# Kernel optimization log

Measured on AMD Instinct MI355X. Metric: run time of the kernel, lower is better.

## Reference

```python
import jax, jax.numpy as jnp
import numpy as np

S, B, N, L, ND = 16, 64, 10000, 128, 1  # seq_len, batch, nodes, latent_dim, node_dim


def setup_inputs() -> dict:
    key = jax.random.key(0)
    ks = jax.random.split(key, 20)
    D_msg = ND + L        # GRU input: [node_feat || time_enc]
    D_h = ND + 2 * L      # attention input: [x || memory || time_enc]
    g = lambda k, shp, s: (jax.random.normal(k, shp, jnp.float32) * s)
    return {
        "x": jax.random.normal(ks[0], (S, B, N, ND), jnp.float32),
        "t": jax.random.uniform(ks[1], (S, B, N, 1), jnp.float32),
        "source": jax.random.randint(ks[2], (S, B, 1), 0, N),
        "target": jax.random.randint(ks[3], (S, B, 1), 0, N),
        "neighbor_mask": jax.random.randint(ks[4], (S, B, N), 0, 2).astype(jnp.bool_),
        # TimeEncoder: cos(t @ w + b)
        "time_w": g(ks[5], (1, L), 1.0),
        "time_b": g(ks[6], (L,), 1.0),
        # MemoryUpdater: GRUCell(input=D_msg, hidden=L)
        "W_ih": g(ks[7], (3 * L, D_msg), 1.0 / np.sqrt(D_msg)),
        "W_hh": g(ks[8], (3 * L, L), 1.0 / np.sqrt(L)),
        "b_ih": jnp.zeros((3 * L,), jnp.float32),
        "b_hh": jnp.zeros((3 * L,), jnp.float32),
        # Attention projections (D_h -> L)
        "Wq": g(ks[9], (D_h, L), 1.0 / np.sqrt(D_h)),
        "bq": jnp.zeros((L,), jnp.float32),
        "Wk": g(ks[10], (D_h, L), 1.0 / np.sqrt(D_h)),
        "bk": jnp.zeros((L,), jnp.float32),
        "Wv": g(ks[11], (D_h, L), 1.0 / np.sqrt(D_h)),
        "bv": jnp.zeros((L,), jnp.float32),
        # final Linear(L -> 1)
        "W_out": g(ks[12], (L, 1), 1.0 / np.sqrt(L)),
        "b_out": jnp.zeros((1,), jnp.float32),
    }


def reference(x, t, source, target, neighbor_mask, time_w, time_b,
              W_ih, W_hh, b_ih, b_hh, Wq, bq, Wk, bk, Wv, bv, W_out, b_out):
    s_len, bsz, n_nodes, _ = x.shape
    lat = time_w.shape[1]
    scale = 1.0 / jnp.sqrt(jnp.float32(lat))
    bidx = jnp.arange(bsz)

    def time_enc(tt):  # [..., 1] -> [..., L]
        return jnp.cos(tt @ time_w + time_b)

    def gru(msg, h):  # torch GRUCell semantics
        gi = msg @ W_ih.T + b_ih
        gh = h @ W_hh.T + b_hh
        i_r, i_z, i_n = jnp.split(gi, 3, axis=-1)
        h_r, h_z, h_n = jnp.split(gh, 3, axis=-1)
        r = jax.nn.sigmoid(i_r + h_r)
        z = jax.nn.sigmoid(i_z + h_z)
        n = jnp.tanh(i_n + r * h_n)
        return (1.0 - z) * n + z * h

    def step(memory, batch):
        xb, tb, src, tgt, mask = batch
        src = src[:, 0]
        tgt = tgt[:, 0]
        dt = time_enc(tb)  # [B, N, L]
        # 1. update memory at source and target nodes
        msg_s = jnp.concatenate([xb[bidx, src], dt[bidx, src]], axis=-1)  # [B, ND+L]
        msg_t = jnp.concatenate([xb[bidx, tgt], dt[bidx, tgt]], axis=-1)
        new_s = gru(msg_s, memory[src])
        new_t = gru(msg_t, memory[tgt])
        mem = memory.at[src].set(new_s).at[tgt].set(new_t)
        # 2. embedding: target query
        tvec = jnp.concatenate([xb[bidx, tgt], mem[tgt]], axis=-1)  # [B, ND+L]
        enc0 = jnp.broadcast_to(jnp.cos(time_b), (bsz, lat))  # time_enc(t=0)
        target_h = jnp.concatenate([tvec, enc0], axis=-1)  # [B, ND+2L]
        # per-node keys/values
        h = jnp.concatenate(
            [xb, jnp.broadcast_to(mem, (bsz, n_nodes, lat)), dt], axis=-1)  # [B, N, ND+2L]
        q = target_h @ Wq + bq          # [B, L]
        k = h @ Wk + bk                 # [B, N, L]
        v = h @ Wv + bv                 # [B, N, L]
        scores = jnp.einsum("bl,bnl->bn", q, k) * scale
        scores = jnp.where(mask, scores, jnp.float32(-1e9))
        attn = jax.nn.softmax(scores, axis=-1)
        z = jnp.einsum("bn,bnl->bl", attn, v)
        logit = z @ W_out + b_out       # [B, 1]
        return mem, logit

    mem0 = jnp.zeros((n_nodes, lat), jnp.float32)
    _, logits = jax.lax.scan(step, mem0, (x, t, source, target, neighbor_mask))
    return logits  # [S, B, 1]
```

## Files before the change

### kernel.cpp

```cpp
#include <hip/hip_runtime.h>
#include <math.h>

#define S_LEN 16
#define BSZ   64
#define NN    10000
#define LAT   128
#define DH    257
#define KTAB  1024
#define CSTRIDE (KTAB + 8)
#define FSTRIDE (KTAB + 4)
#define NTILE 64
#define NTILES 157
#define SCALE 0.08838834764831845f
#define NEG1E9 -1000000000.0f

__global__ __launch_bounds__(256) void setup_all_kernel(
    const float* __restrict__ W_ih, const float* __restrict__ W_hh,
    const float* __restrict__ tw, const float* __restrict__ tb_,
    const float* __restrict__ Wq, const float* __restrict__ bq,
    const float* __restrict__ Wv, const float* __restrict__ bv,
    const float* __restrict__ W_out, const float* __restrict__ b_out,
    const int* __restrict__ mask,
    float* __restrict__ W_ihT, float* __restrict__ W_hhT,
    float* __restrict__ costab, float* __restrict__ wv_out, float* __restrict__ vconst,
    float* __restrict__ qconst, int* __restrict__ modep) {
    int blk = blockIdx.x, tid = threadIdx.x;
    if (blk < 256) {
        int gtid = blk * 256 + tid;
        const int GS = 256 * 256;
        for (int i = gtid; i < 129 * 384; i += GS) { int d = i / 384, j = i % 384; W_ihT[i] = W_ih[j * 129 + d]; }
        for (int i = gtid; i < 128 * 384; i += GS) { int l = i / 384, j = i % 384; W_hhT[i] = W_hh[j * 128 + l]; }
        for (int p = gtid; p <= KTAB; p += GS) {
            float tv = (float)p * (1.0f / KTAB);
            for (int l = 0; l < 128; ++l) costab[l * CSTRIDE + p] = __cosf(tv * tw[l] + tb_[l]);
        }
    } else {
        for (int d = tid; d < DH; d += 256) {
            float a = 0.f;
            for (int j = 0; j < LAT; ++j) a += Wv[d * LAT + j] * W_out[j];
            wv_out[d] = a;
        }
        if (tid == 0) {
            float a = b_out[0];
            for (int j = 0; j < LAT; ++j) a += bv[j] * W_out[j];
            *vconst = a;
        }
        if (tid < 128) {
            float a = bq[tid];
            for (int j = 0; j < 128; ++j) a += __cosf(tb_[j]) * Wq[(129 + j) * LAT + tid];
            qconst[tid] = a;
        }
        __shared__ int hasHigh, hasFloat;
        if (tid == 0) { hasHigh = 0; hasFloat = 0; }
        __syncthreads();
        for (int i = tid; i < 4096; i += 256) {
            int v = mask[i];
            if ((unsigned)v > 1u) atomicOr(&hasHigh, 1);
            if (v == 0x3F800000) atomicOr(&hasFloat, 1);
        }
        __syncthreads();
        if (tid == 0) *modep = hasFloat ? 2 : (hasHigh ? 1 : 0);
    }
}

__global__ __launch_bounds__(256) void setup2_kernel(
    const float* __restrict__ Wk, const float* __restrict__ Wq,
    const float* __restrict__ bk, const float* __restrict__ qconst,
    float* __restrict__ BT, float* __restrict__ uc, float* __restrict__ kw0,
    float* __restrict__ abk, float* __restrict__ scal) {
    int blk = blockIdx.x, tid = threadIdx.x;
    __shared__ float vrow[128];
    if (blk < 128) {
        int l = blk;
        if (tid < 128) vrow[tid] = Wq[(1 + l) * LAT + tid];
        __syncthreads();
        for (int d = tid; d < DH; d += 256) {
            const float* wkr = Wk + d * LAT;
            float a = 0.f;
#pragma unroll 4
            for (int j = 0; j < 128; ++j) a += wkr[j] * vrow[j];
            BT[l * 260 + d] = a;
        }
    } else if (blk == 128) {
        if (tid < 128) vrow[tid] = qconst[tid];
        __syncthreads();
        for (int d = tid; d < DH; d += 256) {
            const float* wkr = Wk + d * LAT;
            float a = 0.f;
#pragma unroll 4
            for (int j = 0; j < 128; ++j) a += wkr[j] * vrow[j];
            uc[d] = a;
        }
    } else if (blk == 129) {
        if (tid < 128) vrow[tid] = Wq[tid];
        __syncthreads();
        for (int d = tid; d < DH; d += 256) {
            const float* wkr = Wk + d * LAT;
            float a = 0.f;
#pragma unroll 4
            for (int j = 0; j < 128; ++j) a += wkr[j] * vrow[j];
            kw0[d] = a;
        }
    } else {
        if (tid < 128) vrow[tid] = bk[tid];
        __syncthreads();
        if (tid < 128) {
            const float* wqr = Wq + (1 + tid) * LAT;
            float a = 0.f;
#pragma unroll 4
            for (int j = 0; j < 128; ++j) a += wqr[j] * vrow[j];
            abk[tid] = a;
        } else if (tid == 128) {
            float a = 0.f;
            for (int j = 0; j < 128; ++j) a += qconst[j] * bk[j];
            scal[0] = a;
        } else if (tid == 129) {
            float a = 0.f;
            for (int j = 0; j < 128; ++j) a += Wq[j] * bk[j];
            scal[1] = a;
        }
    }
}

__device__ __forceinline__ void do_gru_row256(int r, int tid2, int s,
    const float* __restrict__ x, const float* __restrict__ t,
    const int* __restrict__ source, const int* __restrict__ target,
    const float* __restrict__ tw, const float* __restrict__ tb_,
    const float* __restrict__ W_ihT, const float* __restrict__ W_hhT,
    const float* __restrict__ b_ih, const float* __restrict__ b_hh,
    const float* __restrict__ mem, float* __restrict__ newh, float* sm) {
    float* msg = sm;
    float* h   = sm + 132;
    float* gi3 = sm + 260;
    float* gh3 = sm + 644;
    int b = r & 63;
    int idx = (r < 64) ? source[s * BSZ + b] : target[s * BSZ + b];
    const float* xs = x + (size_t)(s * BSZ + b) * NN;
    const float* ts = t + (size_t)(s * BSZ + b) * NN;
    if (tid2 == 0) msg[0] = xs[idx];
    if (tid2 < 128) {
        float tv = ts[idx];
        msg[1 + tid2] = __cosf(tv * tw[tid2] + tb_[tid2]);
        h[tid2] = mem[(size_t)idx * LAT + tid2];
    }
    __syncthreads();
    if (tid2 < 128) {
        int j = tid2;
        float a0 = b_ih[j], a1 = b_ih[128 + j], a2 = b_ih[256 + j];
#pragma unroll 4
        for (int d = 0; d < 129; ++d) {
            float m = msg[d];
            const float* col = W_ihT + d * 384;
            a0 += m * col[j]; a1 += m * col[128 + j]; a2 += m * col[256 + j];
        }
        gi3[j] = a0; gi3[128 + j] = a1; gi3[256 + j] = a2;
    } else {
        int j = tid2 - 128;
        float a0 = b_hh[j], a1 = b_hh[128 + j], a2 = b_hh[256 + j];
#pragma unroll 4
        for (int l = 0; l < 128; ++l) {
            float hv = h[l];
            const float* col = W_hhT + l * 384;
            a0 += hv * col[j]; a1 += hv * col[128 + j]; a2 += hv * col[256 + j];
        }
        gh3[j] = a0; gh3[128 + j] = a1; gh3[256 + j] = a2;
    }
    __syncthreads();
    if (tid2 < 128) {
        int j = tid2;
        float rr = 1.f / (1.f + __expf(-(gi3[j] + gh3[j])));
        float zz = 1.f / (1.f + __expf(-(gi3[128 + j] + gh3[128 + j])));
        float nn2 = tanhf(gi3[256 + j] + rr * gh3[256 + j]);
        newh[r * LAT + j] = (1.f - zz) * nn2 + zz * h[j];
    }
}

__global__ __launch_bounds__(256) void pre_kernel(
    const float* __restrict__ x, const float* __restrict__ t,
    const int* __restrict__ source, const int* __restrict__ target,
    const float* __restrict__ tw, const float* __restrict__ tb_,
    const float* __restrict__ W_ihT, const float* __restrict__ W_hhT,
    const float* __restrict__ b_ih, const float* __restrict__ b_hh,
    const float* __restrict__ mem, float* __restrict__ newh,
    const float* __restrict__ wv_out, const float* __restrict__ costab,
    float* __restrict__ gtab) {
    __shared__ __align__(16) float sm[1028];
    int blk = blockIdx.x, tid = threadIdx.x;
    if (blk < 5) {
        __shared__ float wv_s[LAT];
        if (tid < LAT) wv_s[tid] = wv_out[129 + tid];
        __syncthreads();
        int p = blk * 256 + tid;
        if (p <= KTAB) {
            float a = 0.f;
            for (int l = 0; l < 128; ++l) a += wv_s[l] * costab[l * CSTRIDE + p];
            gtab[p] = a;
        }
        return;
    }
    int r = blk - 5;
    do_gru_row256(r, tid, 0, x, t, source, target, tw, tb_,
                  W_ihT, W_hhT, b_ih, b_hh, mem, newh, sm);
}

__device__ __forceinline__ void do_combine(const float* __restrict__ partials,
                                           const float* __restrict__ vconst,
                                           float* __restrict__ out, int ps, int tid) {
    if (tid >= 64) return;
    int b = tid;
    float M = -3.0e38f, D = 0.f, Nm = 0.f;
    const float4* pp = (const float4*)partials + b * NTILES;
    for (int i = 0; i < NTILES; ++i) {
        float4 p = pp[i];
        float M2 = fmaxf(M, p.x);
        float e1 = __expf(M - M2), e2 = __expf(p.x - M2);
        D = D * e1 + p.y * e2;
        Nm = Nm * e1 + p.z * e2;
        M = M2;
    }
    out[ps * BSZ + b] = Nm / D + vconst[0];
}

__global__ __launch_bounds__(512) void step_a3_kernel(
    const float* __restrict__ x, const int* __restrict__ source, const int* __restrict__ target,
    const float* __restrict__ BT, const float* __restrict__ uc, const float* __restrict__ kw0,
    const float* __restrict__ abk, const float* __restrict__ scal,
    const float* __restrict__ newh, float* __restrict__ mem,
    float* __restrict__ u0_g, float* __restrict__ qbk_g, float* __restrict__ uT,
    float* __restrict__ ftab, const float* __restrict__ costab,
    const float* __restrict__ partials, const float* __restrict__ vconst,
    float* __restrict__ out, int s) {
    int blk = blockIdx.x;
    int tid = threadIdx.x;
    if (blk == 64) {
        __shared__ int idxs[128];
        __shared__ int alive[128];
        if (tid < 128) idxs[tid] = (tid < 64) ? source[s * BSZ + tid] : target[s * BSZ + (tid - 64)];
        __syncthreads();
        if (tid < 128) {
            int i2 = idxs[tid];
            int a = 1;
            for (int r2 = tid + 1; r2 < 128; ++r2)
                if (idxs[r2] == i2) { a = 0; break; }
            alive[tid] = a;
        }
        __syncthreads();
        int row = tid >> 2, q4 = tid & 3;
        if (alive[row]) {
            const float4* srcp = (const float4*)(newh + row * LAT + q4 * 32);
            float4* dstp = (float4*)(mem + (size_t)idxs[row] * LAT + q4 * 32);
#pragma unroll
            for (int j = 0; j < 8; ++j) dstp[j] = srcp[j];
        }
        return;
    }
    if (blk == 65) {
        if (s > 0) do_combine(partials, vconst, out, s - 1, tid);
        return;
    }
    int b = blk;
    __shared__ float memv[128];
    __shared__ float udt_s[128];
    __shared__ float upart[4][260];
    __shared__ float red[8];
    __shared__ __align__(16) float fpart[3 * 1024];
    __shared__ int s_last;
    __shared__ float xvs;
    if (tid < 64) {
        unsigned long long mball = __ballot(target[s * BSZ + tid] == target[s * BSZ + b]);
        if (tid == 0) {
            s_last = 63 - __builtin_clzll(mball);
            xvs = x[(size_t)(s * BSZ + b) * NN + target[s * BSZ + b]];
        }
    }
    __syncthreads();
    if (tid < 128) memv[tid] = newh[(64 + s_last) * LAT + tid];
    __syncthreads();
    float xv = xvs;
    {
        int dd = tid & 127, kc = tid >> 7;
        int l0 = kc * 32;
        for (int d = dd; d < DH; d += 128) {
            float a = 0.f;
#pragma unroll 4
            for (int l = l0; l < l0 + 32; ++l) a += memv[l] * BT[l * 260 + d];
            upart[kc][d] = a;
        }
    }
    __syncthreads();
    if (tid < 257) {
        float a = uc[tid] + xv * kw0[tid] + upart[0][tid] + upart[1][tid] + upart[2][tid] + upart[3][tid];
        if (tid == 0) u0_g[b] = a;
        else if (tid <= 128) uT[(tid - 1) * BSZ + b] = a;
        else udt_s[tid - 129] = a;
    }
    if (tid >= 448) {
        int i = tid - 448;
        float a = memv[i] * abk[i] + memv[64 + i] * abk[64 + i];
        for (int off = 32; off; off >>= 1) a += __shfl_down(a, off, 64);
        if (i == 0) qbk_g[b] = scal[0] + xv * scal[1] + a;
    }
    __syncthreads();
    {
        int pi = tid & 127, lc = tid >> 7;
        int l0 = lc * 32;
        float a0x = 0.f, a0y = 0.f, a0z = 0.f, a0w = 0.f;
        float a1x = 0.f, a1y = 0.f, a1z = 0.f, a1w = 0.f;
#pragma unroll 4
        for (int l = l0; l < l0 + 32; ++l) {
            float ul = udt_s[l];
            const float* cp = &costab[l * CSTRIDE + pi * 8];
            float4 c0 = *(const float4*)cp;
            float4 c1 = *(const float4*)(cp + 4);
            a0x += ul * c0.x; a0y += ul * c0.y; a0z += ul * c0.z; a0w += ul * c0.w;
            a1x += ul * c1.x; a1y += ul * c1.y; a1z += ul * c1.z; a1w += ul * c1.w;
        }
        if (lc) {
            float* fp = &fpart[(lc - 1) * 1024 + pi * 8];
            *(float4*)fp = make_float4(a0x, a0y, a0z, a0w);
            *(float4*)(fp + 4) = make_float4(a1x, a1y, a1z, a1w);
        }
        if (pi == 127) {
            float a = 0.f;
            for (int l = l0; l < l0 + 32; ++l) a += udt_s[l] * costab[l * CSTRIDE + KTAB];
            red[lc] = a;
        }
        __syncthreads();
        if (lc == 0) {
            for (int c = 0; c < 3; ++c) {
                const float* fp = &fpart[c * 1024 + pi * 8];
                a0x += fp[0]; a0y += fp[1]; a0z += fp[2]; a0w += fp[3];
                a1x += fp[4]; a1y += fp[5]; a1z += fp[6]; a1w += fp[7];
            }
            float* fo = &ftab[b * FSTRIDE + pi * 8];
            *(float4*)fo = make_float4(a0x, a0y, a0z, a0w);
            *(float4*)(fo + 4) = make_float4(a1x, a1y, a1z, a1w);
        }
        if (tid == 0) ftab[b * FSTRIDE + KTAB] = red[0] + red[1] + red[2] + red[3];
    }
}

__global__ __launch_bounds__(256) void step_b2_kernel(
    const float* __restrict__ x, const float* __restrict__ t,
    const void* __restrict__ maskp, const int* __restrict__ modep,
    const int* __restrict__ source, const int* __restrict__ target,
    const float* __restrict__ tw, const float* __restrict__ tb_,
    const float* __restrict__ W_ihT, const float* __restrict__ W_hhT,
    const float* __restrict__ b_ih, const float* __restrict__ b_hh,
    const float* __restrict__ mem, float* __restrict__ newh,
    const float* __restrict__ uT, const float* __restrict__ u0_g,
    const float* __restrict__ qbk_g, const float* __restrict__ ftab,
    const float* __restrict__ gtab, const float* __restrict__ wv_out,
    float* __restrict__ partials, int s) {
    int blk = blockIdx.x, tid = threadIdx.x;

    __shared__ float memT[64 * 72];
    __shared__ float uTs[64 * 68];
    __shared__ float memv_s[64];
    __shared__ float wv_s[128];
    __shared__ float u0_s[64], qbk_s[64];

    if (blk >= NTILES) {
        if (s < S_LEN - 1) {
            int r = blk - NTILES;
            do_gru_row256(r, tid, s + 1, x, t, source, target, tw, tb_,
                          W_ihT, W_hhT, b_ih, b_hh, mem, newh, memT );
        }
        return;
    }

    int tile = blk;
    int n0 = tile * NTILE;
    int tb = tid >> 4, tn = tid & 15;
    int nvalid = NN - n0; if (nvalid > NTILE) nvalid = NTILE;

    if (tid < 128) wv_s[tid] = wv_out[1 + tid];
    if (tid < 64) { u0_s[tid] = u0_g[tid]; qbk_s[tid] = qbk_g[tid]; memv_s[tid] = 0.f; }

    float acc[4][4];
#pragma unroll
    for (int i = 0; i < 4; ++i)
#pragma unroll
        for (int j = 0; j < 4; ++j) acc[i][j] = 0.f;

    for (int l0 = 0; l0 < 128; l0 += 64) {
        __syncthreads();
        {
            int n_l = tid & 63, lq = (tid >> 6) * 16;
            if (n_l < nvalid) {
                const float* mrow = mem + (size_t)(n0 + n_l) * LAT + l0 + lq;
                float4 a0 = *(const float4*)(mrow + 0);
                float4 a1 = *(const float4*)(mrow + 4);
                float4 a2 = *(const float4*)(mrow + 8);
                float4 a3 = *(const float4*)(mrow + 12);
                memT[(lq + 0) * 72 + n_l] = a0.x; memT[(lq + 1) * 72 + n_l] = a0.y;
                memT[(lq + 2) * 72 + n_l] = a0.z; memT[(lq + 3) * 72 + n_l] = a0.w;
                memT[(lq + 4) * 72 + n_l] = a1.x; memT[(lq + 5) * 72 + n_l] = a1.y;
                memT[(lq + 6) * 72 + n_l] = a1.z; memT[(lq + 7) * 72 + n_l] = a1.w;
                memT[(lq + 8) * 72 + n_l] = a2.x; memT[(lq + 9) * 72 + n_l] = a2.y;
                memT[(lq + 10) * 72 + n_l] = a2.z; memT[(lq + 11) * 72 + n_l] = a2.w;
                memT[(lq + 12) * 72 + n_l] = a3.x; memT[(lq + 13) * 72 + n_l] = a3.y;
                memT[(lq + 14) * 72 + n_l] = a3.z; memT[(lq + 15) * 72 + n_l] = a3.w;
            } else {
                for (int j = 0; j < 16; ++j) memT[(lq + j) * 72 + n_l] = 0.f;
            }
        }
        {
            int bq4 = (tid & 15) * 4;
            int ll = (tid >> 4) * 4;
            for (int j = 0; j < 4; ++j) {
                float4 v = *(const float4*)&uT[(l0 + ll + j) * BSZ + bq4];
                *(float4*)&uTs[(ll + j) * 68 + bq4] = v;
            }
        }
        __syncthreads();
        if (tid < 64) {
            float a = memv_s[tid];
            for (int l = 0; l < 64; ++l) a += wv_s[l0 + l] * memT[l * 72 + tid];
            memv_s[tid] = a;
        }
        for (int l = 0; l < 64; ++l) {
            float4 uv = *(const float4*)&uTs[l * 68 + tb * 4];
            float4 mv = *(const float4*)&memT[l * 72 + tn * 4];
            acc[0][0] += uv.x * mv.x; acc[0][1] += uv.x * mv.y; acc[0][2] += uv.x * mv.z; acc[0][3] += uv.x * mv.w;
            acc[1][0] += uv.y * mv.x; acc[1][1] += uv.y * mv.y; acc[1][2] += uv.y * mv.z; acc[1][3] += uv.y * mv.w;
            acc[2][0] += uv.z * mv.x; acc[2][1] += uv.z * mv.y; acc[2][2] += uv.z * mv.z; acc[2][3] += uv.z * mv.w;
            acc[3][0] += uv.w * mv.x; acc[3][1] += uv.w * mv.y; acc[3][2] += uv.w * mv.z; acc[3][3] += uv.w * mv.w;
        }
    }
    __syncthreads();

    const float c0 = wv_out[0];
    int mode = *modep;
    const int* m32 = (const int*)maskp;
    const unsigned char* m8 = (const unsigned char*)maskp;
    const float* mf = (const float*)maskp;

    float pm[4], pd[4], pn[4];
#pragma unroll
    for (int i = 0; i < 4; ++i) { pm[i] = -3.0e38f; pd[i] = 0.f; pn[i] = 0.f; }

    for (int i = 0; i < 4; ++i) {
        int b = tb * 4 + i;
        size_t base = (size_t)(s * BSZ + b) * NN + n0 + tn * 4;
        float xv4[4], tv4[4]; int msk[4], vld[4];
        if (tn * 4 + 3 < nvalid) {
            float4 xx = *(const float4*)(x + base);
            float4 tt = *(const float4*)(t + base);
            xv4[0] = xx.x; xv4[1] = xx.y; xv4[2] = xx.z; xv4[3] = xx.w;
            tv4[0] = tt.x; tv4[1] = tt.y; tv4[2] = tt.z; tv4[3] = tt.w;
            if (mode == 1) {
                unsigned mw = *(const unsigned*)(m8 + base);
                msk[0] = mw & 0xff; msk[1] = (mw >> 8) & 0xff; msk[2] = (mw >> 16) & 0xff; msk[3] = (mw >> 24) & 0xff;
            } else if (mode == 2) {
                float4 mm = *(const float4*)(mf + base);
                msk[0] = (mm.x != 0.f); msk[1] = (mm.y != 0.f); msk[2] = (mm.z != 0.f); msk[3] = (mm.w != 0.f);
            } else {
                int4 mm = *(const int4*)(m32 + base);
                msk[0] = mm.x; msk[1] = mm.y; msk[2] = mm.z; msk[3] = mm.w;
            }
            vld[0] = vld[1] = vld[2] = vld[3] = 1;
        } else {
            for (int j = 0; j < 4; ++j) {
                int n = tn * 4 + j;
                vld[j] = (n < nvalid);
                if (vld[j]) {
                    xv4[j] = x[base + j]; tv4[j] = t[base + j];
                    msk[j] = (mode == 1) ? (int)m8[base + j] : (mode == 2) ? (mf[base + j] != 0.f) : m32[base + j];
                } else { xv4[j] = 0.f; tv4[j] = 0.f; msk[j] = 0; }
            }
        }
        const float* ft = ftab + b * FSTRIDE;
#pragma unroll
        for (int j = 0; j < 4; ++j) {
            if (!vld[j]) continue;
            float xv = xv4[j], tv = tv4[j];
            float p = tv * (float)KTAB;
            p = fminf(fmaxf(p, 0.f), (float)KTAB - 0.001f);
            int ii = (int)p;
            float fr = p - (float)ii;
            float f0 = ft[ii];
            float fv = f0 + (ft[ii + 1] - f0) * fr;
            float g0 = gtab[ii];
            float gv = g0 + (gtab[ii + 1] - g0) * fr;
            float sc = SCALE * (xv * u0_s[b] + acc[i][j] + fv + qbk_s[b]);
            if (msk[j] == 0) sc = NEG1E9;
            float val = xv * c0 + memv_s[tn * 4 + j] + gv;
            if (sc > pm[i]) {
                float a = __expf(pm[i] - sc);
                pd[i] = pd[i] * a + 1.f;
                pn[i] = pn[i] * a + val;
                pm[i] = sc;
            } else {
                float e = __expf(sc - pm[i]);
                pd[i] += e;
                pn[i] += e * val;
            }
        }
    }
#pragma unroll
    for (int mk2 = 1; mk2 < 16; mk2 <<= 1) {
#pragma unroll
        for (int i = 0; i < 4; ++i) {
            float mo = __shfl_xor(pm[i], mk2);
            float d2 = __shfl_xor(pd[i], mk2);
            float n2 = __shfl_xor(pn[i], mk2);
            float M = fmaxf(pm[i], mo);
            float e1 = __expf(pm[i] - M), e2 = __expf(mo - M);
            pd[i] = pd[i] * e1 + d2 * e2;
            pn[i] = pn[i] * e1 + n2 * e2;
            pm[i] = M;
        }
    }
    if (tn == 0) {
#pragma unroll
        for (int i = 0; i < 4; ++i) {
            int b = tb * 4 + i;
            *(float4*)&partials[(size_t)(b * NTILES + tile) * 4] = make_float4(pm[i], pd[i], pn[i], 0.f);
        }
    }
}

__global__ __launch_bounds__(64) void tail_kernel(const float* __restrict__ partials,
                                                  const float* __restrict__ vconst,
                                                  float* __restrict__ out) {
    do_combine(partials, vconst, out, S_LEN - 1, threadIdx.x);
}

extern "C" void kernel_launch(void* const* d_in, const int* in_sizes, int n_in,
                              void* d_out, int out_size, void* d_ws, size_t ws_size,
                              hipStream_t stream) {
    const float* x      = (const float*)d_in[0];
    const float* t      = (const float*)d_in[1];
    const int*   source = (const int*)d_in[2];
    const int*   target = (const int*)d_in[3];
    const void*  maskp  = (const void*)d_in[4];
    const float* tw     = (const float*)d_in[5];
    const float* tb     = (const float*)d_in[6];
    const float* W_ih   = (const float*)d_in[7];
    const float* W_hh   = (const float*)d_in[8];
    const float* b_ih   = (const float*)d_in[9];
    const float* b_hh   = (const float*)d_in[10];
    const float* Wq     = (const float*)d_in[11];
    const float* bq     = (const float*)d_in[12];
    const float* Wk     = (const float*)d_in[13];
    const float* bk     = (const float*)d_in[14];
    const float* Wv     = (const float*)d_in[15];
    const float* bv     = (const float*)d_in[16];
    const float* W_out  = (const float*)d_in[17];
    const float* b_out  = (const float*)d_in[18];
    float* out = (float*)d_out;

    float* w = (float*)d_ws;
    float* mem    = w; w += (size_t)NN * LAT;
    float* newh   = w; w += 128 * LAT;
    float* uT     = w; w += LAT * BSZ;
    float* u0_g   = w; w += BSZ;
    float* qbk_g  = w; w += BSZ;
    float* ftab   = w; w += BSZ * FSTRIDE;
    float* gtab   = w; w += FSTRIDE;
    float* costab = w; w += LAT * CSTRIDE;
    float* partials = w; w += (size_t)BSZ * NTILES * 4;
    float* wv_out = w; w += 260;
    float* vconst = w; w += 4;
    float* W_ihT  = w; w += 129 * 384;
    float* W_hhT  = w; w += 128 * 384;
    float* BT     = w; w += 128 * 260;
    float* uc     = w; w += 260;
    float* kw0    = w; w += 260;
    float* abk    = w; w += 128;
    float* qconst = w; w += 128;
    float* scal   = w; w += 8;
    int*   modep  = (int*)w;

    hipMemsetAsync(mem, 0, (size_t)NN * LAT * sizeof(float), stream);
    setup_all_kernel<<<257, 256, 0, stream>>>(W_ih, W_hh, tw, tb, Wq, bq, Wv, bv, W_out, b_out,
                                              (const int*)maskp, W_ihT, W_hhT,
                                              costab, wv_out, vconst, qconst, modep);
    setup2_kernel<<<131, 256, 0, stream>>>(Wk, Wq, bk, qconst, BT, uc, kw0, abk, scal);
    pre_kernel<<<133, 256, 0, stream>>>(x, t, source, target, tw, tb,
                                        W_ihT, W_hhT, b_ih, b_hh, mem, newh,
                                        wv_out, costab, gtab);

    for (int s = 0; s < S_LEN; ++s) {
        step_a3_kernel<<<66, 512, 0, stream>>>(x, source, target, BT, uc, kw0, abk, scal,
                                               newh, mem, u0_g, qbk_g, uT, ftab, costab,
                                               partials, vconst, out, s);
        step_b2_kernel<<<NTILES + 128, 256, 0, stream>>>(x, t, maskp, modep, source, target,
                                                         tw, tb, W_ihT, W_hhT, b_ih, b_hh,
                                                         mem, newh, uT, u0_g, qbk_g,
                                                         ftab, gtab, wv_out, partials, s);
    }
    tail_kernel<<<1, 64, 0, stream>>>(partials, vconst, out);
}
```

Measured before the change: 822.2 us.

## Fuse per-step kernels into one double-buffered step kernel with GRU lookahead

Merges the two per-step kernels into a single step kernel and double-buffers newh, uT, ftab and partials by step parity. This lets the GRU update for the next step run alongside the attention tiles of the current step, and the previous step's updated rows are forwarded by index lookup rather than waiting on a memory scatter. The setup kernels are merged into one, and the final combine is spread over 64 blocks. The aim is to halve the per-step launch count and serialization, at the cost of more complex cross-step data dependencies and races to reason about.

```diff
diff --git a/kernel.cpp b/kernel.cpp
--- a/kernel.cpp
+++ b/kernel.cpp
@@ -11,231 +11,351 @@
 #define FSTRIDE (KTAB + 4)
 #define NTILE 64
 #define NTILES 157
+#define STEP_BLKS 350
 #define SCALE 0.08838834764831845f
 #define NEG1E9 -1000000000.0f
 
-__global__ __launch_bounds__(256) void setup_all_kernel(
-    const float* __restrict__ W_ih, const float* __restrict__ W_hh,
-    const float* __restrict__ tw, const float* __restrict__ tb_,
-    const float* __restrict__ Wq, const float* __restrict__ bq,
-    const float* __restrict__ Wv, const float* __restrict__ bv,
-    const float* __restrict__ W_out, const float* __restrict__ b_out,
-    const int* __restrict__ mask,
-    float* __restrict__ W_ihT, float* __restrict__ W_hhT,
-    float* __restrict__ costab, float* __restrict__ wv_out, float* __restrict__ vconst,
-    float* __restrict__ qconst, int* __restrict__ modep) {
+struct KP {
+    const float *x, *t;
+    const int *source, *target;
+    const void *maskp;
+    const float *tw, *tb_;
+    const float *W_ih, *W_hh, *b_ih, *b_hh;
+    const float *Wq, *bq, *Wk, *bk, *Wv, *bv, *W_out, *b_out;
+    float *out;
+    float *mem;
+    float *newh[2], *uT[2], *u0qbk[2], *ftab[2], *partials[2];
+    float *gtab, *costab;
+    float *wv_out, *vconst, *W_ihT, *W_hhT, *BT, *uc, *kw0, *abk, *scal;
+    int *modep;
+};
+
+__device__ void gru_a_block(const KP& p, float* sm, int r, int snext, int sprev, int zeroH) {
+    int tid = threadIdx.x;
+    int par = snext & 1;
+    float* msg = sm;
+    float* h   = sm + 132;
+    float* gi3 = sm + 260;
+    float* gh3 = sm + 644;
+    float* hn  = sm + 1028;
+    int*   itab = (int*)(sm + 1156);
+    float* axv = sm + 1284;
+    unsigned long long* amask = (unsigned long long*)(sm + 1288);
+    float* udt = sm + 1296;
+    float* red2 = sm + 1424;
+    float* fpart = sm + 1440;
+
+    int b = r & 63;
+    int idx = (r < 64) ? p.source[snext * BSZ + b] : p.target[snext * BSZ + b];
+    if (sprev >= 0 && tid < 128)
+        itab[tid] = (tid < 64) ? p.source[sprev * BSZ + tid] : p.target[sprev * BSZ + (tid - 64)];
+    const float* xs = p.x + (size_t)(snext * BSZ + b) * NN;
+    const float* ts = p.t + (size_t)(snext * BSZ + b) * NN;
+    if (tid == 0) msg[0] = xs[idx];
+    if (tid < 128) {
+        float tv = ts[idx];
+        msg[1 + tid] = __cosf(tv * p.tw[tid] + p.tb_[tid]);
+    }
+    __syncthreads();
+    int w = -1;
+    if (sprev >= 0) {
+        for (int k = 127; k >= 0; --k) if (itab[k] == idx) { w = k; break; }
+    }
+    if (tid < 128) {
+        h[tid] = zeroH ? 0.f
+               : (w >= 0 ? p.newh[par ^ 1][w * LAT + tid] : p.mem[(size_t)idx * LAT + tid]);
+    }
+    __syncthreads();
+    if (tid < 128) {
+        int j = tid;
+        float a0 = p.b_ih[j], a1 = p.b_ih[128 + j], a2 = p.b_ih[256 + j];
+#pragma unroll 4
+        for (int d = 0; d < 129; ++d) {
+            float m = msg[d];
+            const float* col = p.W_ihT + d * 384;
+            a0 += m * col[j]; a1 += m * col[128 + j]; a2 += m * col[256 + j];
+        }
+        gi3[j] = a0; gi3[128 + j] = a1; gi3[256 + j] = a2;
+    } else {
+        int j = tid - 128;
+        float a0 = p.b_hh[j], a1 = p.b_hh[128 + j], a2 = p.b_hh[256 + j];
+#pragma unroll 4
+        for (int l = 0; l < 128; ++l) {
+            float hv = h[l];
+            const float* col = p.W_hhT + l * 384;
+            a0 += hv * col[j]; a1 += hv * col[128 + j]; a2 += hv * col[256 + j];
+        }
+        gh3[j] = a0; gh3[128 + j] = a1; gh3[256 + j] = a2;
+    }
+    __syncthreads();
+    if (tid < 128) {
+        int j = tid;
+        float rr = 1.f / (1.f + __expf(-(gi3[j] + gh3[j])));
+        float zz = 1.f / (1.f + __expf(-(gi3[128 + j] + gh3[128 + j])));
+        float nn2 = tanhf(gi3[256 + j] + rr * gh3[256 + j]);
+        float val = (1.f - zz) * nn2 + zz * h[j];
+        hn[j] = val;
+        p.newh[par][r * LAT + j] = val;
+    }
+    if (r < 64) return;
+
+    int rT = r - 64;
+    int* tg = itab;
+    __syncthreads();
+    if (tid < 64) tg[tid] = p.target[snext * BSZ + tid];
+    __syncthreads();
+    unsigned long long mask = 0;
+    if (tid < 64) {
+        int myt = tg[tid]; int sl = 0;
+        for (int k = 0; k < 64; ++k) if (tg[k] == myt) sl = k;
+        mask = __ballot(sl == rT);
+    }
+    if (tid == 0) *amask = mask;
+    __syncthreads();
+    unsigned long long bl = *amask;
+    float* u0qb = p.u0qbk[par];
+    float* uTb  = p.uT[par];
+    float* ftb  = p.ftab[par];
+    while (bl) {
+        int b2 = __ffsll((long long)bl) - 1; bl &= bl - 1;
+        if (tid == 0) *axv = p.x[(size_t)(snext * BSZ + b2) * NN + tg[b2]];
+        __syncthreads();
+        float xv = *axv;
+        {
+            int d = tid;
+            float a0 = 0.f, a1 = 0.f;
+#pragma unroll 4
+            for (int l = 0; l < 128; l += 2) {
+                a0 += hn[l] * p.BT[l * 260 + d];
+                a1 += hn[l + 1] * p.BT[(l + 1) * 260 + d];
+            }
+            float a = p.uc[d] + xv * p.kw0[d] + a0 + a1;
+            if (d == 0) u0qb[b2] = a;
+            else if (d <= 128) uTb[(d - 1) * BSZ + b2] = a;
+            else udt[d - 129] = a;
+            if (tid == 0) {
+                float c0 = 0.f, c1 = 0.f;
+#pragma unroll 4
+                for (int l = 0; l < 128; l += 2) {
+                    c0 += hn[l] * p.BT[l * 260 + 256];
+                    c1 += hn[l + 1] * p.BT[(l + 1) * 260 + 256];
+                }
+                udt[127] = p.uc[256] + xv * p.kw0[256] + c0 + c1;
+            }
+        }
+        if (tid >= 192) {
+            int i = tid - 192;
+            float a = hn[i] * p.abk[i] + hn[64 + i] * p.abk[64 + i];
+            for (int off = 32; off; off >>= 1) a += __shfl_down(a, off, 64);
+            if (i == 0) u0qb[64 + b2] = p.scal[0] + xv * p.scal[1] + a;
+        }
+        __syncthreads();
+        {
+            int pi = tid & 127, lc = tid >> 7;
+            int l0 = lc * 64;
+            float a0x = 0.f, a0y = 0.f, a0z = 0.f, a0w = 0.f;
+            float a1x = 0.f, a1y = 0.f, a1z = 0.f, a1w = 0.f;
+#pragma unroll 4
+            for (int l = l0; l < l0 + 64; ++l) {
+                float ul = udt[l];
+                const float* cp = &p.costab[l * CSTRIDE + pi * 8];
+                float4 c0 = *(const float4*)cp;
+                float4 c1 = *(const float4*)(cp + 4);
+                a0x += ul * c0.x; a0y += ul * c0.y; a0z += ul * c0.z; a0w += ul * c0.w;
+                a1x += ul * c1.x; a1y += ul * c1.y; a1z += ul * c1.z; a1w += ul * c1.w;
+            }
+            if (lc) {
+                float* fp = &fpart[pi * 8];
+                *(float4*)fp = make_float4(a0x, a0y, a0z, a0w);
+                *(float4*)(fp + 4) = make_float4(a1x, a1y, a1z, a1w);
+            }
+            if (pi == 127) {
+                float a = 0.f;
+                for (int l = l0; l < l0 + 64; ++l) a += udt[l] * p.costab[l * CSTRIDE + KTAB];
+                red2[lc] = a;
+            }
+            __syncthreads();
+            if (lc == 0) {
+                const float* fp = &fpart[pi * 8];
+                a0x += fp[0]; a0y += fp[1]; a0z += fp[2]; a0w += fp[3];
+                a1x += fp[4]; a1y += fp[5]; a1z += fp[6]; a1w += fp[7];
+                float* fo = &ftb[b2 * FSTRIDE + pi * 8];
+                *(float4*)fo = make_float4(a0x, a0y, a0z, a0w);
+                *(float4*)(fo + 4) = make_float4(a1x, a1y, a1z, a1w);
+            }
+            if (tid == 0) ftb[b2 * FSTRIDE + KTAB] = red2[0] + red2[1];
+        }
+        __syncthreads();
+    }
+}
+
+__device__ void combine256(const float* __restrict__ partials, const float* __restrict__ vconst,
+                           float* __restrict__ out, float* sm, int b, int ps) {
+    int tid = threadIdx.x;
+    float m = -3.0e38f, d = 0.f, n = 0.f;
+    if (tid < NTILES) {
+        float4 v = *((const float4*)partials + b * NTILES + tid);
+        m = v.x; d = v.y; n = v.z;
+    }
+#pragma unroll
+    for (int off = 32; off; off >>= 1) {
+        float mo = __shfl_down(m, off, 64);
+        float d2 = __shfl_down(d, off, 64);
+        float n2 = __shfl_down(n, off, 64);
+        float M = fmaxf(m, mo);
+        float e1 = __expf(m - M), e2 = __expf(mo - M);
+        d = d * e1 + d2 * e2; n = n * e1 + n2 * e2; m = M;
+    }
+    float* red = sm;
+    int w = tid >> 6;
+    if ((tid & 63) == 0) { red[w * 3] = m; red[w * 3 + 1] = d; red[w * 3 + 2] = n; }
+    __syncthreads();
+    if (tid == 0) {
+        float M = red[0], D = red[1], Nm = red[2];
+        for (int k2 = 1; k2 < 4; ++k2) {
+            float m2 = red[k2 * 3], d2 = red[k2 * 3 + 1], n2 = red[k2 * 3 + 2];
+            float M2 = fmaxf(M, m2);
+            float e1 = __expf(M - M2), e2 = __expf(m2 - M2);
+            D = D * e1 + d2 * e2; Nm = Nm * e1 + n2 * e2; M = M2;
+        }
+        out[ps * BSZ + b] = Nm / D + vconst[0];
+    }
+}
+
+__global__ __launch_bounds__(256) void setup_kernel(KP p) {
     int blk = blockIdx.x, tid = threadIdx.x;
+    __shared__ float sm[256];
     if (blk < 256) {
         int gtid = blk * 256 + tid;
         const int GS = 256 * 256;
-        for (int i = gtid; i < 129 * 384; i += GS) { int d = i / 384, j = i % 384; W_ihT[i] = W_ih[j * 129 + d]; }
-        for (int i = gtid; i < 128 * 384; i += GS) { int l = i / 384, j = i % 384; W_hhT[i] = W_hh[j * 128 + l]; }
-        for (int p = gtid; p <= KTAB; p += GS) {
-            float tv = (float)p * (1.0f / KTAB);
-            for (int l = 0; l < 128; ++l) costab[l * CSTRIDE + p] = __cosf(tv * tw[l] + tb_[l]);
-        }
-    } else {
+        for (int i = gtid; i < 129 * 384; i += GS) { int d = i / 384, j = i % 384; p.W_ihT[i] = p.W_ih[j * 129 + d]; }
+        for (int i = gtid; i < 128 * 384; i += GS) { int l = i / 384, j = i % 384; p.W_hhT[i] = p.W_hh[j * 128 + l]; }
+        for (int pp = gtid; pp <= KTAB; pp += GS) {
+            float tv = (float)pp * (1.0f / KTAB);
+            for (int l = 0; l < 128; ++l) p.costab[l * CSTRIDE + pp] = __cosf(tv * p.tw[l] + p.tb_[l]);
+        }
+    } else if (blk == 256) {
         for (int d = tid; d < DH; d += 256) {
             float a = 0.f;
-            for (int j = 0; j < LAT; ++j) a += Wv[d * LAT + j] * W_out[j];
-            wv_out[d] = a;
+            for (int j = 0; j < LAT; ++j) a += p.Wv[d * LAT + j] * p.W_out[j];
+            p.wv_out[d] = a;
         }
         if (tid == 0) {
-            float a = b_out[0];
-            for (int j = 0; j < LAT; ++j) a += bv[j] * W_out[j];
-            *vconst = a;
-        }
-        if (tid < 128) {
-            float a = bq[tid];
-            for (int j = 0; j < 128; ++j) a += __cosf(tb_[j]) * Wq[(129 + j) * LAT + tid];
-            qconst[tid] = a;
+            float a = p.b_out[0];
+            for (int j = 0; j < LAT; ++j) a += p.bv[j] * p.W_out[j];
+            p.vconst[0] = a;
         }
         __shared__ int hasHigh, hasFloat;
         if (tid == 0) { hasHigh = 0; hasFloat = 0; }
         __syncthreads();
+        const int* mask = (const int*)p.maskp;
         for (int i = tid; i < 4096; i += 256) {
             int v = mask[i];
             if ((unsigned)v > 1u) atomicOr(&hasHigh, 1);
             if (v == 0x3F800000) atomicOr(&hasFloat, 1);
         }
         __syncthreads();
-        if (tid == 0) *modep = hasFloat ? 2 : (hasHigh ? 1 : 0);
+        if (tid == 0) p.modep[0] = hasFloat ? 2 : (hasHigh ? 1 : 0);
+    } else if (blk < 385) {
+        int l = blk - 257;
+        float* vrow = sm;
+        if (tid < 128) vrow[tid] = p.Wq[(1 + l) * LAT + tid];
+        __syncthreads();
+        for (int d = tid; d < DH; d += 256) {
+            const float* wkr = p.Wk + d * LAT;
+            float a = 0.f;
+#pragma unroll 4
+            for (int j = 0; j < 128; ++j) a += wkr[j] * vrow[j];
+            p.BT[l * 260 + d] = a;
+        }
+    } else if (blk == 385) {
+        float* vrow = sm;
+        if (tid < 128) vrow[tid] = p.Wq[tid];
+        __syncthreads();
+        for (int d = tid; d < DH; d += 256) {
+            const float* wkr = p.Wk + d * LAT;
+            float a = 0.f;
+#pragma unroll 4
+            for (int j = 0; j < 128; ++j) a += wkr[j] * vrow[j];
+            p.kw0[d] = a;
+        }
+    } else if (blk == 386) {
+        __shared__ float cosv[128], qc[128];
+        if (tid < 128) cosv[tid] = __cosf(p.tb_[tid]);
+        __syncthreads();
+        if (tid < 128) {
+            float a = p.bq[tid];
+            for (int j = 0; j < 128; ++j) a += cosv[j] * p.Wq[(129 + j) * LAT + tid];
+            qc[tid] = a;
+        }
+        __syncthreads();
+        for (int d = tid; d < DH; d += 256) {
+            const float* wkr = p.Wk + d * LAT;
+            float a = 0.f;
+#pragma unroll 4
+            for (int j = 0; j < 128; ++j) a += wkr[j] * qc[j];
+            p.uc[d] = a;
+        }
+    } else {
+        __shared__ float bkv[128], cosv[128], tpart[128];
+        if (tid < 128) { bkv[tid] = p.bk[tid]; cosv[tid] = __cosf(p.tb_[tid]); }
+        __syncthreads();
+        if (tid < 128) {
+            const float* wqr = p.Wq + (1 + tid) * LAT;
+            float a = 0.f;
+#pragma unroll 4
+            for (int j = 0; j < 128; ++j) a += wqr[j] * bkv[j];
+            p.abk[tid] = a;
+        } else {
+            int j = tid - 128;
+            const float* wqr = p.Wq + (129 + j) * LAT;
+            float a = 0.f;
+#pragma unroll 4
+            for (int l = 0; l < 128; ++l) a += wqr[l] * bkv[l];
+            tpart[j] = cosv[j] * a;
+        }
+        __syncthreads();
+        if (tid == 0) {
+            float s0 = 0.f, s1 = 0.f;
+            for (int l = 0; l < 128; ++l) { s0 += p.bq[l] * bkv[l]; s1 += p.Wq[l] * bkv[l]; }
+            for (int j = 0; j < 128; ++j) s0 += tpart[j];
+            p.scal[0] = s0; p.scal[1] = s1;
+        }
     }
 }
 
-__global__ __launch_bounds__(256) void setup2_kernel(
-    const float* __restrict__ Wk, const float* __restrict__ Wq,
-    const float* __restrict__ bk, const float* __restrict__ qconst,
-    float* __restrict__ BT, float* __restrict__ uc, float* __restrict__ kw0,
-    float* __restrict__ abk, float* __restrict__ scal) {
-    int blk = blockIdx.x, tid = threadIdx.x;
-    __shared__ float vrow[128];
-    if (blk < 128) {
-        int l = blk;
-        if (tid < 128) vrow[tid] = Wq[(1 + l) * LAT + tid];
-        __syncthreads();
-        for (int d = tid; d < DH; d += 256) {
-            const float* wkr = Wk + d * LAT;
-            float a = 0.f;
-#pragma unroll 4
-            for (int j = 0; j < 128; ++j) a += wkr[j] * vrow[j];
-            BT[l * 260 + d] = a;
-        }
-    } else if (blk == 128) {
-        if (tid < 128) vrow[tid] = qconst[tid];
-        __syncthreads();
-        for (int d = tid; d < DH; d += 256) {
-            const float* wkr = Wk + d * LAT;
-            float a = 0.f;
-#pragma unroll 4
-            for (int j = 0; j < 128; ++j) a += wkr[j] * vrow[j];
-            uc[d] = a;
-        }
-    } else if (blk == 129) {
-        if (tid < 128) vrow[tid] = Wq[tid];
-        __syncthreads();
-        for (int d = tid; d < DH; d += 256) {
-            const float* wkr = Wk + d * LAT;
-            float a = 0.f;
-#pragma unroll 4
-            for (int j = 0; j < 128; ++j) a += wkr[j] * vrow[j];
-            kw0[d] = a;
-        }
-    } else {
-        if (tid < 128) vrow[tid] = bk[tid];
-        __syncthreads();
-        if (tid < 128) {
-            const float* wqr = Wq + (1 + tid) * LAT;
-            float a = 0.f;
-#pragma unroll 4
-            for (int j = 0; j < 128; ++j) a += wqr[j] * vrow[j];
-            abk[tid] = a;
-        } else if (tid == 128) {
-            float a = 0.f;
-            for (int j = 0; j < 128; ++j) a += qconst[j] * bk[j];
-            scal[0] = a;
-        } else if (tid == 129) {
-            float a = 0.f;
-            for (int j = 0; j < 128; ++j) a += Wq[j] * bk[j];
-            scal[1] = a;
-        }
-    }
-}
-
-__device__ __forceinline__ void do_gru_row256(int r, int tid2, int s,
-    const float* __restrict__ x, const float* __restrict__ t,
-    const int* __restrict__ source, const int* __restrict__ target,
-    const float* __restrict__ tw, const float* __restrict__ tb_,
-    const float* __restrict__ W_ihT, const float* __restrict__ W_hhT,
-    const float* __restrict__ b_ih, const float* __restrict__ b_hh,
-    const float* __restrict__ mem, float* __restrict__ newh, float* sm) {
-    float* msg = sm;
-    float* h   = sm + 132;
-    float* gi3 = sm + 260;
-    float* gh3 = sm + 644;
-    int b = r & 63;
-    int idx = (r < 64) ? source[s * BSZ + b] : target[s * BSZ + b];
-    const float* xs = x + (size_t)(s * BSZ + b) * NN;
-    const float* ts = t + (size_t)(s * BSZ + b) * NN;
-    if (tid2 == 0) msg[0] = xs[idx];
-    if (tid2 < 128) {
-        float tv = ts[idx];
-        msg[1 + tid2] = __cosf(tv * tw[tid2] + tb_[tid2]);
-        h[tid2] = mem[(size_t)idx * LAT + tid2];
-    }
-    __syncthreads();
-    if (tid2 < 128) {
-        int j = tid2;
-        float a0 = b_ih[j], a1 = b_ih[128 + j], a2 = b_ih[256 + j];
-#pragma unroll 4
-        for (int d = 0; d < 129; ++d) {
-            float m = msg[d];
-            const float* col = W_ihT + d * 384;
-            a0 += m * col[j]; a1 += m * col[128 + j]; a2 += m * col[256 + j];
-        }
-        gi3[j] = a0; gi3[128 + j] = a1; gi3[256 + j] = a2;
-    } else {
-        int j = tid2 - 128;
-        float a0 = b_hh[j], a1 = b_hh[128 + j], a2 = b_hh[256 + j];
-#pragma unroll 4
-        for (int l = 0; l < 128; ++l) {
-            float hv = h[l];
-            const float* col = W_hhT + l * 384;
-            a0 += hv * col[j]; a1 += hv * col[128 + j]; a2 += hv * col[256 + j];
-        }
-        gh3[j] = a0; gh3[128 + j] = a1; gh3[256 + j] = a2;
-    }
-    __syncthreads();
-    if (tid2 < 128) {
-        int j = tid2;
-        float rr = 1.f / (1.f + __expf(-(gi3[j] + gh3[j])));
-        float zz = 1.f / (1.f + __expf(-(gi3[128 + j] + gh3[128 + j])));
-        float nn2 = tanhf(gi3[256 + j] + rr * gh3[256 + j]);
-        newh[r * LAT + j] = (1.f - zz) * nn2 + zz * h[j];
-    }
-}
-
-__global__ __launch_bounds__(256) void pre_kernel(
-    const float* __restrict__ x, const float* __restrict__ t,
-    const int* __restrict__ source, const int* __restrict__ target,
-    const float* __restrict__ tw, const float* __restrict__ tb_,
-    const float* __restrict__ W_ihT, const float* __restrict__ W_hhT,
-    const float* __restrict__ b_ih, const float* __restrict__ b_hh,
-    const float* __restrict__ mem, float* __restrict__ newh,
-    const float* __restrict__ wv_out, const float* __restrict__ costab,
-    float* __restrict__ gtab) {
-    __shared__ __align__(16) float sm[1028];
+__global__ __launch_bounds__(256) void pre2_kernel(KP p) {
+    __shared__ __align__(16) float sm[2464];
     int blk = blockIdx.x, tid = threadIdx.x;
     if (blk < 5) {
         __shared__ float wv_s[LAT];
-        if (tid < LAT) wv_s[tid] = wv_out[129 + tid];
-        __syncthreads();
-        int p = blk * 256 + tid;
-        if (p <= KTAB) {
+        if (tid < LAT) wv_s[tid] = p.wv_out[129 + tid];
+        __syncthreads();
+        int pp = blk * 256 + tid;
+        if (pp <= KTAB) {
             float a = 0.f;
-            for (int l = 0; l < 128; ++l) a += wv_s[l] * costab[l * CSTRIDE + p];
-            gtab[p] = a;
+            for (int l = 0; l < 128; ++l) a += wv_s[l] * p.costab[l * CSTRIDE + pp];
+            p.gtab[pp] = a;
         }
         return;
     }
-    int r = blk - 5;
-    do_gru_row256(r, tid, 0, x, t, source, target, tw, tb_,
-                  W_ihT, W_hhT, b_ih, b_hh, mem, newh, sm);
+    gru_a_block(p, sm, blk - 5, 0, -1, 1);
 }
 
-__device__ __forceinline__ void do_combine(const float* __restrict__ partials,
-                                           const float* __restrict__ vconst,
-                                           float* __restrict__ out, int ps, int tid) {
-    if (tid >= 64) return;
-    int b = tid;
-    float M = -3.0e38f, D = 0.f, Nm = 0.f;
-    const float4* pp = (const float4*)partials + b * NTILES;
-    for (int i = 0; i < NTILES; ++i) {
-        float4 p = pp[i];
-        float M2 = fmaxf(M, p.x);
-        float e1 = __expf(M - M2), e2 = __expf(p.x - M2);
-        D = D * e1 + p.y * e2;
-        Nm = Nm * e1 + p.z * e2;
-        M = M2;
-    }
-    out[ps * BSZ + b] = Nm / D + vconst[0];
-}
-
-__global__ __launch_bounds__(512) void step_a3_kernel(
-    const float* __restrict__ x, const int* __restrict__ source, const int* __restrict__ target,
-    const float* __restrict__ BT, const float* __restrict__ uc, const float* __restrict__ kw0,
-    const float* __restrict__ abk, const float* __restrict__ scal,
-    const float* __restrict__ newh, float* __restrict__ mem,
-    float* __restrict__ u0_g, float* __restrict__ qbk_g, float* __restrict__ uT,
-    float* __restrict__ ftab, const float* __restrict__ costab,
-    const float* __restrict__ partials, const float* __restrict__ vconst,
-    float* __restrict__ out, int s) {
-    int blk = blockIdx.x;
-    int tid = threadIdx.x;
-    if (blk == 64) {
-        __shared__ int idxs[128];
-        __shared__ int alive[128];
-        if (tid < 128) idxs[tid] = (tid < 64) ? source[s * BSZ + tid] : target[s * BSZ + (tid - 64)];
+__global__ __launch_bounds__(256) void step_kernel(KP p, int s) {
+    __shared__ __align__(16) float sm[9472];
+    int blk = blockIdx.x, tid = threadIdx.x;
+    int par = s & 1;
+
+    if (blk >= 157 && blk < 285) {
+        if (s < S_LEN - 1)
+            gru_a_block(p, sm, blk - 157, s + 1, s, 0);
+        return;
+    }
+    if (blk == 285) {
+        int* idxs  = (int*)sm;
+        int* alive = idxs + 128;
+        if (tid < 128) idxs[tid] = (tid < 64) ? p.source[s * BSZ + tid] : p.target[s * BSZ + (tid - 64)];
         __syncthreads();
         if (tid < 128) {
             int i2 = idxs[tid];
@@ -245,137 +365,46 @@
             alive[tid] = a;
         }
         __syncthreads();
-        int row = tid >> 2, q4 = tid & 3;
+        int row = tid >> 1, q2 = tid & 1;
         if (alive[row]) {
-            const float4* srcp = (const float4*)(newh + row * LAT + q4 * 32);
-            float4* dstp = (float4*)(mem + (size_t)idxs[row] * LAT + q4 * 32);
-#pragma unroll
-            for (int j = 0; j < 8; ++j) dstp[j] = srcp[j];
+            const float4* srcp = (const float4*)(p.newh[par] + row * LAT + q2 * 64);
+            float4* dstp = (float4*)(p.mem + (size_t)idxs[row] * LAT + q2 * 64);
+#pragma unroll
+            for (int j = 0; j < 16; ++j) dstp[j] = srcp[j];
         }
         return;
     }
-    if (blk == 65) {
-        if (s > 0) do_combine(partials, vconst, out, s - 1, tid);
+    if (blk >= 286) {
+        if (s > 0) combine256(p.partials[par ^ 1], p.vconst, p.out, sm, blk - 286, s - 1);
         return;
     }
-    int b = blk;
-    __shared__ float memv[128];
-    __shared__ float udt_s[128];
-    __shared__ float upart[4][260];
-    __shared__ float red[8];
-    __shared__ __align__(16) float fpart[3 * 1024];
-    __shared__ int s_last;
-    __shared__ float xvs;
-    if (tid < 64) {
-        unsigned long long mball = __ballot(target[s * BSZ + tid] == target[s * BSZ + b]);
-        if (tid == 0) {
-            s_last = 63 - __builtin_clzll(mball);
-            xvs = x[(size_t)(s * BSZ + b) * NN + target[s * BSZ + b]];
-        }
-    }
-    __syncthreads();
-    if (tid < 128) memv[tid] = newh[(64 + s_last) * LAT + tid];
-    __syncthreads();
-    float xv = xvs;
-    {
-        int dd = tid & 127, kc = tid >> 7;
-        int l0 = kc * 32;
-        for (int d = dd; d < DH; d += 128) {
-            float a = 0.f;
-#pragma unroll 4
-            for (int l = l0; l < l0 + 32; ++l) a += memv[l] * BT[l * 260 + d];
-            upart[kc][d] = a;
-        }
-    }
-    __syncthreads();
-    if (tid < 257) {
-        float a = uc[tid] + xv * kw0[tid] + upart[0][tid] + upart[1][tid] + upart[2][tid] + upart[3][tid];
-        if (tid == 0) u0_g[b] = a;
-        else if (tid <= 128) uT[(tid - 1) * BSZ + b] = a;
-        else udt_s[tid - 129] = a;
-    }
-    if (tid >= 448) {
-        int i = tid - 448;
-        float a = memv[i] * abk[i] + memv[64 + i] * abk[64 + i];
-        for (int off = 32; off; off >>= 1) a += __shfl_down(a, off, 64);
-        if (i == 0) qbk_g[b] = scal[0] + xv * scal[1] + a;
-    }
-    __syncthreads();
-    {
-        int pi = tid & 127, lc = tid >> 7;
-        int l0 = lc * 32;
-        float a0x = 0.f, a0y = 0.f, a0z = 0.f, a0w = 0.f;
-        float a1x = 0.f, a1y = 0.f, a1z = 0.f, a1w = 0.f;
-#pragma unroll 4
-        for (int l = l0; l < l0 + 32; ++l) {
-            float ul = udt_s[l];
-            const float* cp = &costab[l * CSTRIDE + pi * 8];
-            float4 c0 = *(const float4*)cp;
-            float4 c1 = *(const float4*)(cp + 4);
-            a0x += ul * c0.x; a0y += ul * c0.y; a0z += ul * c0.z; a0w += ul * c0.w;
-            a1x += ul * c1.x; a1y += ul * c1.y; a1z += ul * c1.z; a1w += ul * c1.w;
-        }
-        if (lc) {
-            float* fp = &fpart[(lc - 1) * 1024 + pi * 8];
-            *(float4*)fp = make_float4(a0x, a0y, a0z, a0w);
-            *(float4*)(fp + 4) = make_float4(a1x, a1y, a1z, a1w);
-        }
-        if (pi == 127) {
-            float a = 0.f;
-            for (int l = l0; l < l0 + 32; ++l) a += udt_s[l] * costab[l * CSTRIDE + KTAB];
-            red[lc] = a;
-        }
-        __syncthreads();
-        if (lc == 0) {
-            for (int c = 0; c < 3; ++c) {
-                const float* fp = &fpart[c * 1024 + pi * 8];
-                a0x += fp[0]; a0y += fp[1]; a0z += fp[2]; a0w += fp[3];
-                a1x += fp[4]; a1y += fp[5]; a1z += fp[6]; a1w += fp[7];
-            }
-            float* fo = &ftab[b * FSTRIDE + pi * 8];
-            *(float4*)fo = make_float4(a0x, a0y, a0z, a0w);
-            *(float4*)(fo + 4) = make_float4(a1x, a1y, a1z, a1w);
-        }
-        if (tid == 0) ftab[b * FSTRIDE + KTAB] = red[0] + red[1] + red[2] + red[3];
-    }
-}
-
-__global__ __launch_bounds__(256) void step_b2_kernel(
-    const float* __restrict__ x, const float* __restrict__ t,
-    const void* __restrict__ maskp, const int* __restrict__ modep,
-    const int* __restrict__ source, const int* __restrict__ target,
-    const float* __restrict__ tw, const float* __restrict__ tb_,
-    const float* __restrict__ W_ihT, const float* __restrict__ W_hhT,
-    const float* __restrict__ b_ih, const float* __restrict__ b_hh,
-    const float* __restrict__ mem, float* __restrict__ newh,
-    const float* __restrict__ uT, const float* __restrict__ u0_g,
-    const float* __restrict__ qbk_g, const float* __restrict__ ftab,
-    const float* __restrict__ gtab, const float* __restrict__ wv_out,
-    float* __restrict__ partials, int s) {
-    int blk = blockIdx.x, tid = threadIdx.x;
-
-    __shared__ float memT[64 * 72];
-    __shared__ float uTs[64 * 68];
-    __shared__ float memv_s[64];
-    __shared__ float wv_s[128];
-    __shared__ float u0_s[64], qbk_s[64];
-
-    if (blk >= NTILES) {
-        if (s < S_LEN - 1) {
-            int r = blk - NTILES;
-            do_gru_row256(r, tid, s + 1, x, t, source, target, tw, tb_,
-                          W_ihT, W_hhT, b_ih, b_hh, mem, newh, memT );
-        }
-        return;
-    }
-
+
+    float* memT   = sm;
+    float* uTs    = sm + 4608;
+    float* memv_s = sm + 8960;
+    float* wv_s   = sm + 9024;
+    float* u0_s   = sm + 9152;
+    float* qbk_s  = sm + 9216;
+    int*   idxs   = (int*)(sm + 9280);
+    int*   prow   = idxs + 128;
     int tile = blk;
     int n0 = tile * NTILE;
     int tb = tid >> 4, tn = tid & 15;
     int nvalid = NN - n0; if (nvalid > NTILE) nvalid = NTILE;
 
-    if (tid < 128) wv_s[tid] = wv_out[1 + tid];
-    if (tid < 64) { u0_s[tid] = u0_g[tid]; qbk_s[tid] = qbk_g[tid]; memv_s[tid] = 0.f; }
+    if (tid < 128) wv_s[tid] = p.wv_out[1 + tid];
+    if (tid < 64) {
+        u0_s[tid] = p.u0qbk[par][tid];
+        qbk_s[tid] = p.u0qbk[par][64 + tid];
+        memv_s[tid] = 0.f;
+    }
+    if (tid < 128) idxs[tid] = (tid < 64) ? p.source[s * BSZ + tid] : p.target[s * BSZ + (tid - 64)];
+    __syncthreads();
+    if (tid < 64) {
+        int node = n0 + tid; int w = -1;
+        for (int k = 127; k >= 0; --k) if (idxs[k] == node) { w = k; break; }
+        prow[tid] = w;
+    }
 
     float acc[4][4];
 #pragma unroll
@@ -383,12 +412,15 @@
 #pragma unroll
         for (int j = 0; j < 4; ++j) acc[i][j] = 0.f;
 
+    const float* nh = p.newh[par];
     for (int l0 = 0; l0 < 128; l0 += 64) {
         __syncthreads();
         {
             int n_l = tid & 63, lq = (tid >> 6) * 16;
             if (n_l < nvalid) {
-                const float* mrow = mem + (size_t)(n0 + n_l) * LAT + l0 + lq;
+                int w = prow[n_l];
+                const float* mrow = (w >= 0) ? (nh + w * LAT + l0 + lq)
+                                             : (p.mem + (size_t)(n0 + n_l) * LAT + l0 + lq);
                 float4 a0 = *(const float4*)(mrow + 0);
                 float4 a1 = *(const float4*)(mrow + 4);
                 float4 a2 = *(const float4*)(mrow + 8);
@@ -408,8 +440,9 @@
         {
             int bq4 = (tid & 15) * 4;
             int ll = (tid >> 4) * 4;
+            const float* uTb = p.uT[par];
             for (int j = 0; j < 4; ++j) {
-                float4 v = *(const float4*)&uT[(l0 + ll + j) * BSZ + bq4];
+                float4 v = *(const float4*)&uTb[(l0 + ll + j) * BSZ + bq4];
                 *(float4*)&uTs[(ll + j) * 68 + bq4] = v;
             }
         }
@@ -430,11 +463,13 @@
     }
     __syncthreads();
 
-    const float c0 = wv_out[0];
-    int mode = *modep;
-    const int* m32 = (const int*)maskp;
-    const unsigned char* m8 = (const unsigned char*)maskp;
-    const float* mf = (const float*)maskp;
+    const float c0 = p.wv_out[0];
+    int mode = p.modep[0];
+    const int* m32 = (const int*)p.maskp;
+    const unsigned char* m8 = (const unsigned char*)p.maskp;
+    const float* mf = (const float*)p.maskp;
+    const float* gtab = p.gtab;
+    const float* ftb = p.ftab[par];
 
     float pm[4], pd[4], pn[4];
 #pragma unroll
@@ -445,8 +480,8 @@
         size_t base = (size_t)(s * BSZ + b) * NN + n0 + tn * 4;
         float xv4[4], tv4[4]; int msk[4], vld[4];
         if (tn * 4 + 3 < nvalid) {
-            float4 xx = *(const float4*)(x + base);
-            float4 tt = *(const float4*)(t + base);
+            float4 xx = *(const float4*)(p.x + base);
+            float4 tt = *(const float4*)(p.t + base);
             xv4[0] = xx.x; xv4[1] = xx.y; xv4[2] = xx.z; xv4[3] = xx.w;
             tv4[0] = tt.x; tv4[1] = tt.y; tv4[2] = tt.z; tv4[3] = tt.w;
             if (mode == 1) {
@@ -465,20 +500,20 @@
                 int n = tn * 4 + j;
                 vld[j] = (n < nvalid);
                 if (vld[j]) {
-                    xv4[j] = x[base + j]; tv4[j] = t[base + j];
+                    xv4[j] = p.x[base + j]; tv4[j] = p.t[base + j];
                     msk[j] = (mode == 1) ? (int)m8[base + j] : (mode == 2) ? (mf[base + j] != 0.f) : m32[base + j];
                 } else { xv4[j] = 0.f; tv4[j] = 0.f; msk[j] = 0; }
             }
         }
-        const float* ft = ftab + b * FSTRIDE;
+        const float* ft = ftb + b * FSTRIDE;
 #pragma unroll
         for (int j = 0; j < 4; ++j) {
             if (!vld[j]) continue;
             float xv = xv4[j], tv = tv4[j];
-            float p = tv * (float)KTAB;
-            p = fminf(fmaxf(p, 0.f), (float)KTAB - 0.001f);
-            int ii = (int)p;
-            float fr = p - (float)ii;
+            float pq = tv * (float)KTAB;
+            pq = fminf(fmaxf(pq, 0.f), (float)KTAB - 0.001f);
+            int ii = (int)pq;
+            float fr = pq - (float)ii;
             float f0 = ft[ii];
             float fv = f0 + (ft[ii + 1] - f0) * fr;
             float g0 = gtab[ii];
@@ -516,80 +551,70 @@
 #pragma unroll
         for (int i = 0; i < 4; ++i) {
             int b = tb * 4 + i;
-            *(float4*)&partials[(size_t)(b * NTILES + tile) * 4] = make_float4(pm[i], pd[i], pn[i], 0.f);
+            *(float4*)&p.partials[par][(size_t)(b * NTILES + tile) * 4] = make_float4(pm[i], pd[i], pn[i], 0.f);
         }
     }
 }
 
-__global__ __launch_bounds__(64) void tail_kernel(const float* __restrict__ partials,
-                                                  const float* __restrict__ vconst,
-                                                  float* __restrict__ out) {
-    do_combine(partials, vconst, out, S_LEN - 1, threadIdx.x);
+__global__ __launch_bounds__(256) void tail2_kernel(KP p) {
+    __shared__ float sm[16];
+    combine256(p.partials[(S_LEN - 1) & 1], p.vconst, p.out, sm, blockIdx.x, S_LEN - 1);
 }
 
 extern "C" void kernel_launch(void* const* d_in, const int* in_sizes, int n_in,
                               void* d_out, int out_size, void* d_ws, size_t ws_size,
                               hipStream_t stream) {
-    const float* x      = (const float*)d_in[0];
-    const float* t      = (const float*)d_in[1];
-    const int*   source = (const int*)d_in[2];
-    const int*   target = (const int*)d_in[3];
-    const void*  maskp  = (const void*)d_in[4];
-    const float* tw     = (const float*)d_in[5];
-    const float* tb     = (const float*)d_in[6];
-    const float* W_ih   = (const float*)d_in[7];
-    const float* W_hh   = (const float*)d_in[8];
-    const float* b_ih   = (const float*)d_in[9];
-    const float* b_hh   = (const float*)d_in[10];
-    const float* Wq     = (const float*)d_in[11];
-    const float* bq     = (const float*)d_in[12];
-    const float* Wk     = (const float*)d_in[13];
-    const float* bk     = (const float*)d_in[14];
-    const float* Wv     = (const float*)d_in[15];
-    const float* bv     = (const float*)d_in[16];
-    const float* W_out  = (const float*)d_in[17];
-    const float* b_out  = (const float*)d_in[18];
-    float* out = (float*)d_out;
+    KP kp;
+    kp.x      = (const float*)d_in[0];
+    kp.t      = (const float*)d_in[1];
+    kp.source = (const int*)d_in[2];
+    kp.target = (const int*)d_in[3];
+    kp.maskp  = (const void*)d_in[4];
+    kp.tw     = (const float*)d_in[5];
+    kp.tb_    = (const float*)d_in[6];
+    kp.W_ih   = (const float*)d_in[7];
+    kp.W_hh   = (const float*)d_in[8];
+    kp.b_ih   = (const float*)d_in[9];
+    kp.b_hh   = (const float*)d_in[10];
+    kp.Wq     = (const float*)d_in[11];
+    kp.bq     = (const float*)d_in[12];
+    kp.Wk     = (const float*)d_in[13];
+    kp.bk     = (const float*)d_in[14];
+    kp.Wv     = (const float*)d_in[15];
+    kp.bv     = (const float*)d_in[16];
+    kp.W_out  = (const float*)d_in[17];
+    kp.b_out  = (const float*)d_in[18];
+    kp.out    = (float*)d_out;
 
     float* w = (float*)d_ws;
-    float* mem    = w; w += (size_t)NN * LAT;
-    float* newh   = w; w += 128 * LAT;
-    float* uT     = w; w += LAT * BSZ;
-    float* u0_g   = w; w += BSZ;
-    float* qbk_g  = w; w += BSZ;
-    float* ftab   = w; w += BSZ * FSTRIDE;
-    float* gtab   = w; w += FSTRIDE;
-    float* costab = w; w += LAT * CSTRIDE;
-    float* partials = w; w += (size_t)BSZ * NTILES * 4;
-    float* wv_out = w; w += 260;
-    float* vconst = w; w += 4;
-    float* W_ihT  = w; w += 129 * 384;
-    float* W_hhT  = w; w += 128 * 384;
-    float* BT     = w; w += 128 * 260;
-    float* uc     = w; w += 260;
-    float* kw0    = w; w += 260;
-    float* abk    = w; w += 128;
-    float* qconst = w; w += 128;
-    float* scal   = w; w += 8;
-    int*   modep  = (int*)w;
-
-    hipMemsetAsync(mem, 0, (size_t)NN * LAT * sizeof(float), stream);
-    setup_all_kernel<<<257, 256, 0, stream>>>(W_ih, W_hh, tw, tb, Wq, bq, Wv, bv, W_out, b_out,
-                                              (const int*)maskp, W_ihT, W_hhT,
-                                              costab, wv_out, vconst, qconst, modep);
-    setup2_kernel<<<131, 256, 0, stream>>>(Wk, Wq, bk, qconst, BT, uc, kw0, abk, scal);
-    pre_kernel<<<133, 256, 0, stream>>>(x, t, source, target, tw, tb,
-                                        W_ihT, W_hhT, b_ih, b_hh, mem, newh,
-                                        wv_out, costab, gtab);
-
-    for (int s = 0; s < S_LEN; ++s) {
-        step_a3_kernel<<<66, 512, 0, stream>>>(x, source, target, BT, uc, kw0, abk, scal,
-                                               newh, mem, u0_g, qbk_g, uT, ftab, costab,
-                                               partials, vconst, out, s);
-        step_b2_kernel<<<NTILES + 128, 256, 0, stream>>>(x, t, maskp, modep, source, target,
-                                                         tw, tb, W_ihT, W_hhT, b_ih, b_hh,
-                                                         mem, newh, uT, u0_g, qbk_g,
-                                                         ftab, gtab, wv_out, partials, s);
-    }
-    tail_kernel<<<1, 64, 0, stream>>>(partials, vconst, out);
+    kp.mem        = w; w += (size_t)NN * LAT;
+    kp.newh[0]    = w; w += 128 * LAT;
+    kp.newh[1]    = w; w += 128 * LAT;
+    kp.uT[0]      = w; w += LAT * BSZ;
+    kp.uT[1]      = w; w += LAT * BSZ;
+    kp.u0qbk[0]   = w; w += 128;
+    kp.u0qbk[1]   = w; w += 128;
+    kp.ftab[0]    = w; w += BSZ * FSTRIDE;
+    kp.ftab[1]    = w; w += BSZ * FSTRIDE;
+    kp.partials[0] = w; w += (size_t)BSZ * NTILES * 4;
+    kp.partials[1] = w; w += (size_t)BSZ * NTILES * 4;
+    kp.gtab       = w; w += 1056;
+    kp.costab     = w; w += LAT * CSTRIDE;
+    kp.wv_out     = w; w += 288;
+    kp.vconst     = w; w += 32;
+    kp.W_ihT      = w; w += 129 * 384;
+    kp.W_hhT      = w; w += 128 * 384;
+    kp.BT         = w; w += 128 * 260;
+    kp.uc         = w; w += 288;
+    kp.kw0        = w; w += 288;
+    kp.abk        = w; w += 128;
+    kp.scal       = w; w += 32;
+    kp.modep      = (int*)w; w += 32;
+
+    hipMemsetAsync(kp.mem, 0, (size_t)NN * LAT * sizeof(float), stream);
+    setup_kernel<<<388, 256, 0, stream>>>(kp);
+    pre2_kernel<<<133, 256, 0, stream>>>(kp);
+    for (int s = 0; s < S_LEN; ++s)
+        step_kernel<<<STEP_BLKS, 256, 0, stream>>>(kp, s);
+    tail2_kernel<<<64, 256, 0, stream>>>(kp);
 }
```

Result: no change. 832.2 us (+1.2%).
